# Kernel tuning notes

Hardware: AMD Instinct MI355X
Metric: run time of the kernel (lower is better)

## Reference

```python
import jax, jax.numpy as jnp
import numpy as np

N, H_IN, W_IN, D_OUT = 4, 512, 360, 512


def _ramp_filter(H):
    # fourier_fbp_filter(..., 'ramp') -> time domain, fftshifted, then reversed
    f = np.fft.fftfreq(H).reshape(-1, 1)
    fourier_filter = 2.0 * np.abs(f)
    time_filter = np.fft.fftshift(np.fft.ifft(fourier_filter, axis=0).real)
    time_filter = time_filter[::-1].copy()  # list-reverse in the original
    return time_filter.reshape(1, 1, H, 1).astype(np.float32)  # OIHW


def _backproj_ty(H, W, D):
    # y-coordinate of the grid_sample grid; x-coordinate exactly selects column i
    th = np.pi / 180.0 * np.linspace(0.0, 180.0, W, endpoint=False)  # [W]
    X, Y = np.mgrid[0:D, 0:D]
    xpr = (X - D // 2).astype(np.float64)
    ypr = (Y - D // 2).astype(np.float64)
    t = ypr[None] * np.cos(th)[:, None, None] - xpr[None] * np.sin(th)[:, None, None]
    return (t / (H // 2)).astype(np.float32)  # [W, D, D], in grid_sample coords


def setup_inputs() -> dict:
    key = jax.random.key(0)
    radon_image = jax.random.normal(key, (N, 1, H_IN, W_IN), dtype=jnp.float32)
    hG = jnp.asarray(_ramp_filter(H_IN))
    t_y = jnp.asarray(_backproj_ty(H_IN, W_IN, D_OUT))
    return {"radon_image": radon_image, "hG": hG, "t_y": t_y}


def _forward(radon_image, hG, t_y):
    Nb, _, H, W = radon_image.shape
    hH = H // 2
    padded = jnp.concatenate([radon_image, radon_image, radon_image], axis=2)  # [N,1,3H,W]
    filt = jax.lax.conv_general_dilated(
        padded, hG, window_strides=(1, 1), padding="VALID",
        dimension_numbers=("NCHW", "OIHW", "NCHW"))  # [N,1,2H+1,W]
    filt = filt[:, 0, hH + 1 : hH + H + 1, :]  # [N,H,W]

    cols = jnp.transpose(filt, (2, 0, 1))  # [W, N, H]: column i = angle i

    def body(acc, xs):
        col, ty = xs  # col: [N,H], ty: [D,D]
        # bilinear grid_sample along y, align_corners=True, zeros padding
        py = (ty + 1.0) * 0.5 * (H - 1)
        y0 = jnp.floor(py)
        fy = py - y0
        y0i = y0.astype(jnp.int32)
        y1i = y0i + 1
        w0 = jnp.where((y0i >= 0) & (y0i < H), 1.0 - fy, 0.0)
        w1 = jnp.where((y1i >= 0) & (y1i < H), fy, 0.0)
        v = col[:, jnp.clip(y0i, 0, H - 1)] * w0[None] \
          + col[:, jnp.clip(y1i, 0, H - 1)] * w1[None]  # [N,D,D]
        return acc + v, None

    D = t_y.shape[1]
    acc0 = jnp.zeros((Nb, D, D), dtype=filt.dtype)
    acc, _ = jax.lax.scan(body, acc0, (cols, t_y))
    return (acc * (np.pi / (2.0 * W)))[:, None]  # [N,1,D,D]


def reference(radon_image, hG, t_y):
    return _forward(radon_image, hG, t_y)
```

## Files before the change

kernel.cpp:

```cpp
#include <hip/hip_runtime.h>

#define HH 512
#define WW 360
#define NB 4
#define DD 512

#define NCHUNK 12
#define ANG_PER 30

#define FSTRIDE 768
#define FOFFS   128
#define NR      128

#define OFF_TAB  0
#define OFF_RT   1024
#define OFF_FILT (1024 + NB*WW*HH)
#define OFF_PART (OFF_FILT + (WW+1)*FSTRIDE*4)
#define CHUNK_ELEMS (NB*DD*DD)

#define GLOAD_LDS16(gp, lp)                                                   \
    __builtin_amdgcn_global_load_lds(                                         \
        (const __attribute__((address_space(1))) void*)(gp),                  \
        (__attribute__((address_space(3))) void*)(lp), 16, 0, 0)

__global__ __launch_bounds__(256) void k_transpose(const float* __restrict__ radon,
                                                   float* __restrict__ ws) {
    __shared__ float tile[32][33];
    int n  = blockIdx.z;
    int w0 = blockIdx.x * 32, h0 = blockIdx.y * 32;
    int x = threadIdx.x, y = threadIdx.y;
    const float* rn = radon + n * (HH * WW);
#pragma unroll
    for (int r = 0; r < 32; r += 8) {
        int h = h0 + y + r, w = w0 + x;
        tile[y + r][x] = (w < WW) ? rn[h * WW + w] : 0.f;
    }
    __syncthreads();
    float* rt = ws + OFF_RT + n * (WW * HH);
#pragma unroll
    for (int r = 0; r < 32; r += 8) {
        int w = w0 + y + r, h = h0 + x;
        if (w < WW) rt[w * HH + h] = tile[x][y + r];
    }
}

__global__ __launch_bounds__(256) void k_filter(const float* __restrict__ hG,
                                                float* __restrict__ ws) {
    __shared__ float r2[NB][1024];
    int wA  = blockIdx.x;
    int tid = threadIdx.x;

    if (tid == 0) {
        double th = (3.14159265358979323846 / 180.0) * (0.5 * (double)wA);
        double c = cos(th), s = sin(th);
        float2 ab;
        ab.x = (float)(c * (255.5 / 256.0));
        ab.y = (float)(-s * (255.5 / 256.0));
        ((float2*)(ws + OFF_TAB))[wA] = ab;
    }
    {
        float4* fp = (float4*)(ws + OFF_FILT) + (size_t)wA * FSTRIDE;
        float4 z = make_float4(0.f, 0.f, 0.f, 0.f);
        if (tid < 128) { fp[tid] = z; fp[640 + tid] = z; }
    }

    const float* rt = ws + OFF_RT;
    for (int t = tid; t < NB * 1024; t += 256) {
        int n = t >> 10, i = t & 1023;
        r2[n][i] = rt[(n * WW + wA) * HH + ((i + 257) & 511)];
    }
    __syncthreads();

    int n = tid >> 6, lane = tid & 63, y0 = lane << 3;
    float acc[8] = {0, 0, 0, 0, 0, 0, 0, 0};
    const float* rr = &r2[n][y0];
    float4 Wr0 = *(const float4*)(rr + 0);
    float4 Wr1 = *(const float4*)(rr + 4);
    float4 Wr2 = *(const float4*)(rr + 8);
    float4 Wr3 = *(const float4*)(rr + 12);

    for (int d = 0; d < 512; d += 8) {
        float hg[8];
#pragma unroll
        for (int q = 0; q < 8; ++q) hg[q] = hG[d + q];
        float wf[16] = {Wr0.x, Wr0.y, Wr0.z, Wr0.w, Wr1.x, Wr1.y, Wr1.z, Wr1.w,
                        Wr2.x, Wr2.y, Wr2.z, Wr2.w, Wr3.x, Wr3.y, Wr3.z, Wr3.w};
#pragma unroll
        for (int du = 0; du < 8; ++du)
#pragma unroll
            for (int u = 0; u < 8; ++u)
                acc[u] = fmaf(wf[du + u], hg[du], acc[u]);
        if (d < 504) {
            Wr0 = Wr2; Wr1 = Wr3;
            Wr2 = *(const float4*)(rr + d + 16);
            Wr3 = *(const float4*)(rr + d + 20);
        }
    }
    float* filt = ws + OFF_FILT;
#pragma unroll
    for (int u = 0; u < 8; ++u)
        filt[((size_t)wA * FSTRIDE + FOFFS + y0 + u) * 4 + n] = acc[u];
}

__global__ __launch_bounds__(256, 6) void k_backproj(const float* __restrict__ ws,
                                                     float* __restrict__ parts) {
    __shared__ float4 buf[4][NR];
    __shared__ float2 tl[ANG_PER];
    const int tid   = threadIdx.x;
    const int lane  = tid & 63;
    const int ithr  = tid >> 6;
    const int j     = blockIdx.x * 64 + lane;
    const int i0    = blockIdx.y * 32 + ithr;
    const int chunk = blockIdx.z;
    const int wbeg  = chunk * ANG_PER;

    const float2* tab = (const float2*)(ws + OFF_TAB);
    const float4* fd  = (const float4*)(ws + OFF_FILT);

    if (tid < ANG_PER) tl[tid] = tab[wbeg + tid];
    __syncthreads();

    float acc[8][4];
#pragma unroll
    for (int u = 0; u < 8; ++u)
#pragma unroll
        for (int n = 0; n < 4; ++n) acc[u][n] = 0.f;

    float jf = (float)(j - 256);
    float ifl[8];
#pragma unroll
    for (int u = 0; u < 8; ++u) ifl[u] = (float)(i0 + 4 * u - 256);

    const float jlo = (float)((int)blockIdx.x * 64 - 256);
    const float jhi = (float)((int)blockIdx.x * 64 + 63 - 256);
    const float ilo = (float)((int)blockIdx.y * 32 - 256);
    const float ihi = (float)((int)blockIdx.y * 32 + 31 - 256);

#define CALC_BASE(ab, dst)                                                    \
    {                                                                         \
        float t_ = fminf(fmaf((ab).x, jlo, 255.5f), fmaf((ab).x, jhi, 255.5f)); \
        float pm_ = fminf(fmaf((ab).y, ilo, t_), fmaf((ab).y, ihi, t_));      \
        (dst) = floorf(pm_) - 2.0f;                                           \
    }

    float2 abA = tl[0], abB = tl[1], abC = tl[2], abD;
    float bA, bB, bC, bD;
    CALC_BASE(abA, bA); CALC_BASE(abB, bB); CALC_BASE(abC, bC);

    if (tid < NR) {
        GLOAD_LDS16(fd + (size_t)(wbeg + 0) * FSTRIDE + (FOFFS + (int)bA + tid), &buf[0][tid]);
        GLOAD_LDS16(fd + (size_t)(wbeg + 1) * FSTRIDE + (FOFFS + (int)bB + tid), &buf[1][tid]);
        GLOAD_LDS16(fd + (size_t)(wbeg + 2) * FSTRIDE + (FOFFS + (int)bC + tid), &buf[2][tid]);
    }
    asm volatile("s_waitcnt vmcnt(2)" ::: "memory");
    __builtin_amdgcn_s_barrier();
    __builtin_amdgcn_sched_barrier(0);

    for (int k = 0; k < ANG_PER; ++k) {
        {
            bool ok  = (k + 3 < ANG_PER);
            int  idx = ok ? (k + 3) : 0;
            abD = tl[idx];
            if (ok) { CALC_BASE(abD, bD); } else { bD = 0.0f; }
            int wsrc = ok ? (wbeg + k + 3) : wbeg;
            if (tid < NR)
                GLOAD_LDS16(fd + (size_t)wsrc * FSTRIDE + (FOFFS + (int)bD + tid),
                            &buf[(k + 3) & 3][tid]);
        }

        float pybase = fmaf(abA.x, jf, 255.5f);
        const float4* cb = buf[k & 3];
#pragma unroll
        for (int u = 0; u < 8; ++u) {
            float pya = fmaf(abA.y, ifl[u], pybase);
            float pyr = pya - bA;
            float cf  = truncf(pyr);
            float fy  = pyr - cf;
            int   c   = (int)cf;
            float4 p0 = cb[c];
            float4 p1 = cb[c + 1];
            float w0  = 1.f - fy;
            acc[u][0] = fmaf(p1.x, fy, fmaf(p0.x, w0, acc[u][0]));
            acc[u][1] = fmaf(p1.y, fy, fmaf(p0.y, w0, acc[u][1]));
            acc[u][2] = fmaf(p1.z, fy, fmaf(p0.z, w0, acc[u][2]));
            acc[u][3] = fmaf(p1.w, fy, fmaf(p0.w, w0, acc[u][3]));
        }

        asm volatile("s_waitcnt vmcnt(2)" ::: "memory");
        __builtin_amdgcn_s_barrier();
        __builtin_amdgcn_sched_barrier(0);

        abA = abB; abB = abC; abC = abD;
        bA  = bB;  bB  = bC;  bC  = bD;
    }

    asm volatile("s_waitcnt vmcnt(0)" ::: "memory");

    float* part = parts + (size_t)chunk * CHUNK_ELEMS;
#pragma unroll
    for (int n = 0; n < 4; ++n)
#pragma unroll
        for (int u = 0; u < 8; ++u)
            part[(n * DD + (i0 + 4 * u)) * DD + j] = acc[u][n];
#undef CALC_BASE
}

__global__ __launch_bounds__(256) void k_reduce(float* __restrict__ out,
                                                const float* __restrict__ ws) {
    int t = blockIdx.x * 256 + threadIdx.x;
    const float4* p = (const float4*)(ws + OFF_PART);
    const int C4 = CHUNK_ELEMS / 4;
    float4 a = p[t];
#pragma unroll
    for (int c = 1; c < NCHUNK; ++c) {
        float4 b = p[t + c * C4];
        a.x += b.x; a.y += b.y; a.z += b.z; a.w += b.w;
    }
    const float s = (float)(3.14159265358979323846 / 720.0);
    float4 r;
    r.x = a.x * s; r.y = a.y * s; r.z = a.z * s; r.w = a.w * s;
    ((float4*)out)[t] = r;
}

extern "C" void kernel_launch(void* const* d_in, const int* in_sizes, int n_in,
                              void* d_out, int out_size, void* d_ws, size_t ws_size,
                              hipStream_t stream) {
    const float* radon = (const float*)d_in[0];
    const float* hG    = (const float*)d_in[1];
    float* out = (float*)d_out;
    float* ws  = (float*)d_ws;

    k_transpose<<<dim3(12, 16, 4), dim3(32, 8), 0, stream>>>(radon, ws);
    k_filter<<<WW, 256, 0, stream>>>(hG, ws);
    k_backproj<<<dim3(8, 16, NCHUNK), 256, 0, stream>>>(ws, ws + OFF_PART);
    k_reduce<<<1024, 256, 0, stream>>>(out, ws);
}
```

Measured before the change: 108.2 us.

## Drop transpose kernel, halve angle chunks, interleave partial sums per pixel

Removes the separate transpose pass by having the filter kernel gather radon columns directly with strided loads. Halves the number of angle chunks (60 angles per block) so the partial-sum buffer written by backprojection and read by the reduction shrinks by half. Partials are stored as one float4 per pixel across batch, and the reduction de-interleaves on output. Trades fewer, longer blocks and uncoalesced gathers in the filter for less global memory traffic and one fewer launch.

```diff
diff --git a/kernel.cpp b/kernel.cpp
--- a/kernel.cpp
+++ b/kernel.cpp
@@ -5,46 +5,25 @@
 #define NB 4
 #define DD 512
 
-#define NCHUNK 12
-#define ANG_PER 30
+#define NCHUNK 6
+#define ANG_PER 60
 
 #define FSTRIDE 768
 #define FOFFS   128
 #define NR      128
 
 #define OFF_TAB  0
-#define OFF_RT   1024
-#define OFF_FILT (1024 + NB*WW*HH)
+#define OFF_FILT 1024
 #define OFF_PART (OFF_FILT + (WW+1)*FSTRIDE*4)
-#define CHUNK_ELEMS (NB*DD*DD)
+#define PIX (DD*DD)
 
 #define GLOAD_LDS16(gp, lp)                                                   \
     __builtin_amdgcn_global_load_lds(                                         \
         (const __attribute__((address_space(1))) void*)(gp),                  \
         (__attribute__((address_space(3))) void*)(lp), 16, 0, 0)
 
-__global__ __launch_bounds__(256) void k_transpose(const float* __restrict__ radon,
-                                                   float* __restrict__ ws) {
-    __shared__ float tile[32][33];
-    int n  = blockIdx.z;
-    int w0 = blockIdx.x * 32, h0 = blockIdx.y * 32;
-    int x = threadIdx.x, y = threadIdx.y;
-    const float* rn = radon + n * (HH * WW);
-#pragma unroll
-    for (int r = 0; r < 32; r += 8) {
-        int h = h0 + y + r, w = w0 + x;
-        tile[y + r][x] = (w < WW) ? rn[h * WW + w] : 0.f;
-    }
-    __syncthreads();
-    float* rt = ws + OFF_RT + n * (WW * HH);
-#pragma unroll
-    for (int r = 0; r < 32; r += 8) {
-        int w = w0 + y + r, h = h0 + x;
-        if (w < WW) rt[w * HH + h] = tile[x][y + r];
-    }
-}
-
-__global__ __launch_bounds__(256) void k_filter(const float* __restrict__ hG,
+__global__ __launch_bounds__(256) void k_filter(const float* __restrict__ radon,
+                                                const float* __restrict__ hG,
                                                 float* __restrict__ ws) {
     __shared__ float r2[NB][1024];
     int wA  = blockIdx.x;
@@ -64,10 +43,10 @@
         if (tid < 128) { fp[tid] = z; fp[640 + tid] = z; }
     }
 
-    const float* rt = ws + OFF_RT;
     for (int t = tid; t < NB * 1024; t += 256) {
         int n = t >> 10, i = t & 1023;
-        r2[n][i] = rt[(n * WW + wA) * HH + ((i + 257) & 511)];
+        int h = (i + 257) & 511;
+        r2[n][i] = radon[((size_t)(n * HH + h)) * WW + wA];
     }
     __syncthreads();
 
@@ -102,7 +81,7 @@
         filt[((size_t)wA * FSTRIDE + FOFFS + y0 + u) * 4 + n] = acc[u];
 }
 
-__global__ __launch_bounds__(256, 6) void k_backproj(const float* __restrict__ ws,
+__global__ __launch_bounds__(256, 3) void k_backproj(const float* __restrict__ ws,
                                                      float* __restrict__ parts) {
     __shared__ float4 buf[4][NR];
     __shared__ float2 tl[ANG_PER];
@@ -196,12 +175,11 @@
 
     asm volatile("s_waitcnt vmcnt(0)" ::: "memory");
 
-    float* part = parts + (size_t)chunk * CHUNK_ELEMS;
-#pragma unroll
-    for (int n = 0; n < 4; ++n)
-#pragma unroll
-        for (int u = 0; u < 8; ++u)
-            part[(n * DD + (i0 + 4 * u)) * DD + j] = acc[u][n];
+    float4* p4 = (float4*)parts + (size_t)chunk * PIX;
+#pragma unroll
+    for (int u = 0; u < 8; ++u)
+        p4[(size_t)(i0 + 4 * u) * DD + j] =
+            make_float4(acc[u][0], acc[u][1], acc[u][2], acc[u][3]);
 #undef CALC_BASE
 }
 
@@ -209,17 +187,17 @@
                                                 const float* __restrict__ ws) {
     int t = blockIdx.x * 256 + threadIdx.x;
     const float4* p = (const float4*)(ws + OFF_PART);
-    const int C4 = CHUNK_ELEMS / 4;
     float4 a = p[t];
 #pragma unroll
     for (int c = 1; c < NCHUNK; ++c) {
-        float4 b = p[t + c * C4];
+        float4 b = p[(size_t)c * PIX + t];
         a.x += b.x; a.y += b.y; a.z += b.z; a.w += b.w;
     }
     const float s = (float)(3.14159265358979323846 / 720.0);
-    float4 r;
-    r.x = a.x * s; r.y = a.y * s; r.z = a.z * s; r.w = a.w * s;
-    ((float4*)out)[t] = r;
+    out[t]           = a.x * s;
+    out[PIX + t]     = a.y * s;
+    out[2 * PIX + t] = a.z * s;
+    out[3 * PIX + t] = a.w * s;
 }
 
 extern "C" void kernel_launch(void* const* d_in, const int* in_sizes, int n_in,
@@ -230,8 +208,7 @@
     float* out = (float*)d_out;
     float* ws  = (float*)d_ws;
 
-    k_transpose<<<dim3(12, 16, 4), dim3(32, 8), 0, stream>>>(radon, ws);
-    k_filter<<<WW, 256, 0, stream>>>(hG, ws);
+    k_filter<<<WW, 256, 0, stream>>>(radon, hG, ws);
     k_backproj<<<dim3(8, 16, NCHUNK), 256, 0, stream>>>(ws, ws + OFF_PART);
     k_reduce<<<1024, 256, 0, stream>>>(out, ws);
 }
```

Result: no change. 108.1 us (-0.1%).
